# Optimization experiments

Measured on AMD Instinct MI355X. Metric: run time of the kernel, lower is better.

The kernel has to match this reference:

```python
import jax, jax.numpy as jnp
import numpy as np

N = 64
K_CHEB = 5
EPS = 1e-5

# db4 decomposition filters (scaling_filter.mat Lo_D / Hi_D, length 8)
_LO = np.array([-0.010597401784997278, 0.032883011666982945, 0.030841381835986965,
                -0.18703481171888114, -0.02798376941698385, 0.6308807679295904,
                0.7148465705525415, 0.23037781330885523], dtype=np.float32)
_HI = np.array([-0.23037781330885523, 0.7148465705525415, -0.6308807679295904,
                -0.02798376941698385, 0.18703481171888114, 0.030841381835986965,
                0.032883011666982945, -0.010597401784997278], dtype=np.float32)
# torch stores np.flip(filters) and Conv2d does cross-correlation -> use flipped taps here too
_KERN = np.stack([_LO[::-1], _HI[::-1]])[:, None, None, :].copy()  # [2,1,1,8]


def _wavelet_step(x):
    # x: [B, C, 1, W]; circular pad 3 each side, depthwise len-8 conv, stride 2
    p = 3  # filter_length // 2 - 1
    xp = jnp.concatenate([x[..., -p:], x, x[..., :p]], axis=-1)
    b, c, h, wp = xp.shape
    out = jax.lax.conv_general_dilated(
        xp.reshape(b * c, 1, h, wp), jnp.asarray(_KERN), (1, 2), 'VALID',
        dimension_numbers=('NCHW', 'OIHW', 'NCHW'))
    out = out.reshape(b, c, 2, h, -1)
    return out[:, :, 0], out[:, :, 1]  # (approx, detail)


def _cbam(x, fc1, fc2, sa_w):
    # x: [B, 657, 1, 64]; channel attention then spatial attention
    def mlp(v):  # v: [B, C, 1, 1]
        h = jax.nn.relu(jnp.einsum('oc,bchw->bohw', fc1, v))
        return jnp.einsum('oc,bchw->bohw', fc2, h)
    avg = x.mean(axis=(2, 3), keepdims=True)
    mx = x.max(axis=(2, 3), keepdims=True)
    x = x * jax.nn.sigmoid(mlp(avg) + mlp(mx))
    s = jnp.concatenate([x.mean(axis=1, keepdims=True), x.max(axis=1, keepdims=True)], axis=1)
    sa = jax.nn.sigmoid(jax.lax.conv_general_dilated(
        s, sa_w, (1, 1), ((3, 3), (3, 3)), dimension_numbers=('NCHW', 'OIHW', 'NCHW')))
    return x * sa


def _global_edge_weight(w_tril, mask):
    xs, ys = np.tril_indices(N)
    E = jnp.zeros((N, N), w_tril.dtype).at[xs, ys].set(w_tril)
    E = E + E.T - jnp.diag(jnp.diag(E))
    return (E * mask).reshape(-1)


def _norm_adj(edges, w):
    # PyG NewSGConv.norm: add remaining self-loops (fill=1), deg from |w|, sym normalize
    row, col = edges[0], edges[1]
    has_self = jnp.zeros((N,), w.dtype).at[row].add(jnp.where(row == col, 1.0, 0.0)) > 0
    w_self = jnp.where(has_self, 0.0, 1.0).astype(w.dtype)
    deg = jnp.zeros((N,), w.dtype).at[row].add(jnp.abs(w)) + w_self
    dsafe = jnp.where(deg > 0, deg, 1.0)
    dinv = jnp.where(deg > 0, jax.lax.rsqrt(dsafe), 0.0)
    norm = dinv[row] * w * dinv[col]
    A = jnp.zeros((N, N), w.dtype).at[col, row].add(norm)  # out[i] = sum_j A[i,j] x[j]
    return A + jnp.diag(dinv * w_self * dinv)


def _gcn_block(x, A, W, b, g, be):
    # x: [B, N, C_in]; K-hop SGConv propagation, linear, train-mode batchnorm over (B, N)
    for _ in range(K_CHEB):
        x = jnp.einsum('ij,bjc->bic', A, x)
    x = x @ W.T + b
    mean = x.mean(axis=(0, 1))
    var = x.var(axis=(0, 1))
    return (x - mean) * jax.lax.rsqrt(var + EPS) * g + be


def _classify(x, W1, b1, g, be, W2, b2):
    out = x.reshape(x.shape[0], -1) @ W1.T + b1
    out = (out - out.mean(0)) * jax.lax.rsqrt(out.var(0) + EPS) * g + be
    return jax.nn.log_softmax(out @ W2.T + b2, axis=1)


def _forward(x, local_graph_weight, global_mask, ca_fc1, ca_fc2, sa_conv, edge_weight_tril,
             ld_W, ld_b, ld_g, ld_be, ld1_W, ld1_b, ld1_g, ld1_be,
             d_W, d_b, d_g, d_be, d1_W, d1_b, d1_g, d1_be,
             cls_W1, cls_b1, cls_g, cls_be, cls_W2, cls_b2, edges):
    xc = jnp.transpose(x, (0, 3, 2, 1))        # [B, 657, 1, 64]
    xc = _cbam(xc, ca_fc1, ca_fc2, sa_conv)
    xh = jnp.transpose(xc, (0, 3, 2, 1))       # [B, 64, 1, 657]
    # fi = floor(log2(200)) = 7 -> 4 decomposition levels: 657->328->164->82->41
    out1, _gamma = _wavelet_step(xh)
    out2, _beta = _wavelet_step(out1)
    out3, _alpha = _wavelet_step(out2)
    delta, _theta = _wavelet_step(out3)        # [B, 64, 1, 41]
    delta = delta[:, :, 0, :]                  # squeeze -> [B, 64, 41]
    gw = _global_edge_weight(edge_weight_tril, global_mask)
    A_loc = _norm_adj(edges, local_graph_weight)
    A_glb = _norm_adj(edges, gw)
    lf = _gcn_block(delta, A_loc, ld_W, ld_b, ld_g, ld_be)
    lf = _gcn_block(lf, A_loc, ld1_W, ld1_b, ld1_g, ld1_be)
    gf = _gcn_block(delta, A_glb, d_W, d_b, d_g, d_be)
    gf = _gcn_block(gf, A_glb, d1_W, d1_b, d1_g, d1_be)
    feat = jnp.concatenate([lf.mean(-1, keepdims=True), gf.mean(-1, keepdims=True)], axis=2)  # [B,64,2]
    return _classify(feat, cls_W1, cls_b1, cls_g, cls_be, cls_W2, cls_b2)


def setup_inputs() -> dict:
    key = jax.random.key(0)
    ks = iter(jax.random.split(key, 16))
    B = 512
    f32 = jnp.float32
    def rn(shape, s=0.05):
        return jax.random.normal(next(ks), shape, f32) * s
    ii = jnp.arange(N, dtype=jnp.int32)
    edges = jnp.stack([jnp.repeat(ii, N), jnp.tile(ii, N)])  # full 64x64 mesh (incl. self loops)
    return dict(
        x=jax.random.normal(next(ks), (B, N, 1, 657), f32),
        local_graph_weight=jax.random.uniform(next(ks), (N * N,), f32),
        global_mask=jnp.ones((N, N), f32),
        ca_fc1=rn((82, 657)),
        ca_fc2=rn((657, 82)),
        sa_conv=rn((1, 2, 7, 7), 0.1),
        edge_weight_tril=jax.random.uniform(next(ks), (N * (N + 1) // 2,), f32),
        ld_W=rn((16, 41)), ld_b=jnp.zeros(16, f32), ld_g=jnp.ones(16, f32), ld_be=jnp.zeros(16, f32),
        ld1_W=rn((4, 16)), ld1_b=jnp.zeros(4, f32), ld1_g=jnp.ones(4, f32), ld1_be=jnp.zeros(4, f32),
        d_W=rn((16, 41)), d_b=jnp.zeros(16, f32), d_g=jnp.ones(16, f32), d_be=jnp.zeros(16, f32),
        d1_W=rn((4, 16)), d1_b=jnp.zeros(4, f32), d1_g=jnp.ones(4, f32), d1_be=jnp.zeros(4, f32),
        cls_W1=rn((32, 128)), cls_b1=jnp.zeros(32, f32), cls_g=jnp.ones(32, f32), cls_be=jnp.zeros(32, f32),
        cls_W2=rn((2, 32)), cls_b2=jnp.zeros(2, f32),
        edges=edges,
    )


def reference(x, local_graph_weight, global_mask, ca_fc1, ca_fc2, sa_conv, edge_weight_tril,
              ld_W, ld_b, ld_g, ld_be, ld1_W, ld1_b, ld1_g, ld1_be,
              d_W, d_b, d_g, d_be, d1_W, d1_b, d1_g, d1_be,
              cls_W1, cls_b1, cls_g, cls_be, cls_W2, cls_b2, edges):
    return _forward(x, local_graph_weight, global_mask, ca_fc1, ca_fc2, sa_conv, edge_weight_tril,
                    ld_W, ld_b, ld_g, ld_be, ld1_W, ld1_b, ld1_g, ld1_be,
                    d_W, d_b, d_g, d_be, d1_W, d1_b, d1_g, d1_be,
                    cls_W1, cls_b1, cls_g, cls_be, cls_W2, cls_b2, edges)
```

## Files before the change

kernel.cpp:

```cpp
#include <hip/hip_runtime.h>
#include <math.h>

#define NB 512
#define NN 64
#define TL 657
#define LV1 328
#define LV2 164
#define LV3 82
#define LV4 41
#define HID 82
#define ST 66

#define WS_M      0
#define WS_ACC    32768
#define WS_SMEAN  36864
#define WS_SMAX   167936
#define WS_FC2T   299008
#define WS_CSUM   682496
#define WS_CMAX   2028032
#define WS_CATT   3373568
#define WS_Y1     682496
#define WS_DELTA  4876800
#define WS_Y2     4876800
#define WS_OUT1   5925376

#define ACC_Y1 0
#define ACC_Y2 64
#define ACC_O1 80

__device__ __forceinline__ float sigmoidf_(float v){ return 1.0f/(1.0f+expf(-v)); }

__device__ __forceinline__ void wav_level(float* __restrict__ dst, const float* __restrict__ src,
                                          int outL, int inL, int lane){
  const float DLO[8] = {0.23037781330885523f, 0.7148465705525415f, 0.6308807679295904f,
                        -0.02798376941698385f, -0.18703481171888114f, 0.030841381835986965f,
                        0.032883011666982945f, -0.010597401784997278f};
  for (int k=lane; k<outL; k+=64){
    int i0 = 2*k - 3;
    float a = 0.f;
    #pragma unroll
    for (int j=0;j<8;j++){
      int idx = i0 + j;
      idx = (idx < 0) ? idx + inL : ((idx >= inL) ? idx - inL : idx);
      a += src[idx]*DLO[j];
    }
    dst[k] = a;
  }
}

__device__ __forceinline__ void mm8(float* __restrict__ D, int dstride,
                                    const float* __restrict__ A, const float* __restrict__ Bm){
  int tid = threadIdx.x;
  int wv = tid >> 6, lane = tid & 63;
  int i0 = wv*8;
  float acc8[8];
  #pragma unroll
  for (int i=0;i<8;i++) acc8[i]=0.f;
  #pragma unroll
  for (int kc=0; kc<4; kc++){
    float bb[16];
    #pragma unroll
    for (int j=0;j<16;j++) bb[j] = Bm[(kc*16+j)*ST + lane];
    #pragma unroll
    for (int i=0;i<8;i++){
      const float2* ar = (const float2*)&A[(i0+i)*ST + kc*16];
      float s0=0.f, s1=0.f;
      #pragma unroll
      for (int j2=0;j2<8;j2++){
        float2 v = ar[j2];
        s0 += v.x*bb[2*j2]; s1 += v.y*bb[2*j2+1];
      }
      acc8[i] += s0+s1;
    }
  }
  #pragma unroll
  for (int i=0;i<8;i++) D[(i0+i)*dstride + lane] = acc8[i];
}

__global__ __launch_bounds__(512) void k_front(
    const float* __restrict__ x,
    const float* __restrict__ lgw, const float* __restrict__ gmask,
    const float* __restrict__ tril, const int* __restrict__ edges,
    const float* __restrict__ fc2,
    float* __restrict__ csum, float* __restrict__ cmax,
    float* __restrict__ Mout, float* __restrict__ fc2T,
    double* __restrict__ acc)
{
  __shared__ float smem[3*NN*ST];
  __shared__ float deg[64], hs[64], dinv[64], wself[64];
  int tid = threadIdx.x;
  int bid = blockIdx.x;

  if (bid < 2*NB){
    int b = bid >> 1, band = bid & 1;
    int c0   = band ? 329 : 0;
    int len  = band ? 328 : 329;
    if (tid >= len) return;
    int col = c0 + tid;
    const float* p = x + (size_t)b*NN*TL + col;
    float s = 0.f, m = -INFINITY;
    for (int n=0;n<NN;n+=16){
      float v0 = p[0*TL],  v1 = p[1*TL],  v2 = p[2*TL],  v3 = p[3*TL];
      float v4 = p[4*TL],  v5 = p[5*TL],  v6 = p[6*TL],  v7 = p[7*TL];
      float v8 = p[8*TL],  v9 = p[9*TL],  vA = p[10*TL], vB = p[11*TL];
      float vC = p[12*TL], vD = p[13*TL], vE = p[14*TL], vF = p[15*TL];
      p += 16*TL;
      s += ((v0+v1)+(v2+v3)) + ((v4+v5)+(v6+v7)) + ((v8+v9)+(vA+vB)) + ((vC+vD)+(vE+vF));
      float m01 = fmaxf(fmaxf(v0,v1), fmaxf(v2,v3));
      float m23 = fmaxf(fmaxf(v4,v5), fmaxf(v6,v7));
      float m45 = fmaxf(fmaxf(v8,v9), fmaxf(vA,vB));
      float m67 = fmaxf(fmaxf(vC,vD), fmaxf(vE,vF));
      m = fmaxf(m, fmaxf(fmaxf(m01,m23), fmaxf(m45,m67)));
    }
    csum[(size_t)b*TL + col] = s;
    cmax[(size_t)b*TL + col] = m;
    return;
  }

  int gi = bid - 2*NB;
  if (gi >= 2){
    int t8 = gi - 2;
    int r0 = t8*83;
    int rn = (t8==7) ? (TL - 7*83) : 83;
    for (int i=tid; i<rn*HID; i+=512){
      int r = i / HID, u = i - r*HID;
      smem[u*85 + r] = fc2[(size_t)r0*HID + i];
    }
    __syncthreads();
    for (int j=tid; j<HID*83; j+=512){
      int u = j / 83, c = j - u*83;
      if (c < rn) fc2T[u*TL + r0 + c] = smem[u*85 + c];
    }
    return;
  }

  float* Wbuf = smem;
  float* Amat = smem + NN*ST;
  float* P1   = smem + 2*NN*ST;
  int g = gi;
  if (g==0 && tid<512) acc[tid]=0.0;
  for (int e=tid;e<4096;e+=512){
    float w;
    if (g==0) w = lgw[e];
    else {
      int i=e>>6, j=e&63;
      int aa = (i>j)? i:j, bb = (i>j)? j:i;
      w = tril[aa*(aa+1)/2 + bb] * gmask[e];
    }
    Wbuf[e] = w;
  }
  for (int i=tid;i<NN*ST;i+=512) Amat[i] = 0.f;
  if (tid<64){ deg[tid]=0.f; hs[tid]=0.f; }
  __syncthreads();
  {
    int e0 = tid*8;
    int runr = edges[e0];
    float runv = 0.f;
    #pragma unroll 4
    for (int i=0;i<8;i++){
      int e = e0+i;
      int r = edges[e];
      int c = edges[4096+e];
      float w = Wbuf[e];
      if (r != runr){ atomicAdd(&deg[runr], runv); runr = r; runv = 0.f; }
      runv += fabsf(w);
      if (r == c) hs[r] = 1.f;
    }
    atomicAdd(&deg[runr], runv);
  }
  __syncthreads();
  if (tid<64){
    float w_ = (hs[tid] > 0.f) ? 0.f : 1.f;
    float d = deg[tid] + w_;
    dinv[tid] = (d > 0.f) ? rsqrtf(d) : 0.f;
    wself[tid] = w_;
  }
  __syncthreads();
  for (int e=tid;e<4096;e+=512){
    int r = edges[e], c = edges[4096+e];
    float nm = dinv[r]*Wbuf[e]*dinv[c];
    atomicAdd(&Amat[c*ST+r], nm);
  }
  __syncthreads();
  if (tid<64) Amat[tid*ST+tid] += dinv[tid]*wself[tid]*dinv[tid];
  __syncthreads();
  mm8(P1,   ST, Amat, Amat); __syncthreads();
  mm8(Wbuf, ST, P1,   P1);   __syncthreads();
  mm8(&Mout[g*4096], 64, Wbuf, Amat);
}

__global__ __launch_bounds__(512) void k_mlp(
    const float* __restrict__ csum, const float* __restrict__ cmax,
    const float* __restrict__ fc1, const float* __restrict__ fc2T,
    float* __restrict__ catt)
{
  __shared__ float cs[TL], cm[TL];
  __shared__ float h[HID];
  int tid = threadIdx.x, b = blockIdx.x;
  for (int i=tid;i<TL;i+=512){
    cs[i] = csum[(size_t)b*TL + i];
    cm[i] = cmax[(size_t)b*TL + i];
  }
  __syncthreads();
  int wv = tid>>6, lane = tid&63;
  for (int o=wv; o<HID; o+=8){
    const float* fr = fc1 + (size_t)o*TL;
    float a = 0.f, bm = 0.f;
    #pragma unroll
    for (int i=0;i<11;i++){
      int c = lane + 64*i;
      if (c < TL){
        float f = fr[c];
        a += f*cs[c]; bm += f*cm[c];
      }
    }
    #pragma unroll
    for (int off=32;off;off>>=1){
      a  += __shfl_xor(a,off);
      bm += __shfl_xor(bm,off);
    }
    if (lane==0)
      h[o] = fmaxf(a*(1.0f/64.0f),0.f) + fmaxf(bm,0.f);
  }
  __syncthreads();
  for (int c=tid;c<TL;c+=512){
    float a=0.f;
    #pragma unroll 4
    for (int u=0;u<HID;u++) a += fc2T[(size_t)u*TL + c]*h[u];
    catt[(size_t)b*TL + c] = sigmoidf_(a);
  }
}

__global__ __launch_bounds__(256) void k_wav(
    const float* __restrict__ x, const float* __restrict__ catt_g,
    float* __restrict__ delta, float* __restrict__ smean, float* __restrict__ smax)
{
  __shared__ float catt[TL];
  __shared__ float yb[4][TL];
  __shared__ float o1b[4][LV1];
  __shared__ float o2b[4][LV2];
  __shared__ float o3b[4][LV3];
  int tid = threadIdx.x, b = blockIdx.x;
  for (int i=tid;i<TL;i+=256) catt[i] = catt_g[(size_t)b*TL + i];
  __syncthreads();
  int wv = tid>>6, lane = tid&63;
  int n = blockIdx.y*4 + wv;
  float* y  = yb[wv];
  float* p1 = o1b[wv];
  float* p2 = o2b[wv];
  float* p3 = o3b[wv];
  const float DLO[8] = {0.23037781330885523f, 0.7148465705525415f, 0.6308807679295904f,
                        -0.02798376941698385f, -0.18703481171888114f, 0.030841381835986965f,
                        0.032883011666982945f, -0.010597401784997278f};
  const float* row = x + ((size_t)b*NN + n)*TL;
  float ls = 0.f, lm = -INFINITY;
  #pragma unroll
  for (int i=0;i<11;i++){
    int t = lane + 64*i;
    if (t < TL){
      float v = row[t]*catt[t];
      y[t] = v; ls += v; lm = fmaxf(lm,v);
    }
  }
  #pragma unroll
  for (int off=32;off;off>>=1){
    ls += __shfl_xor(ls,off);
    lm = fmaxf(lm, __shfl_xor(lm,off));
  }
  if (lane==0){ smean[b*NN+n] = ls*(1.0f/657.0f); smax[b*NN+n] = lm; }
  wav_level(p1, y,  LV1, TL,  lane);
  wav_level(p2, p1, LV2, LV1, lane);
  wav_level(p3, p2, LV3, LV2, lane);
  if (lane < LV4){
    int i0 = 2*lane - 3;
    float a = 0.f;
    #pragma unroll
    for (int j=0;j<8;j++){
      int idx = i0 + j;
      idx = (idx < 0) ? idx + LV3 : ((idx >= LV3) ? idx - LV3 : idx);
      a += p3[idx]*DLO[j];
    }
    delta[((size_t)b*NN + n)*LV4 + lane] = a;
  }
}

__global__ __launch_bounds__(256) void k_gcn1(
  const float* __restrict__ delta, const float* __restrict__ Mmat,
  const float* __restrict__ smean, const float* __restrict__ smax,
  const float* __restrict__ saw,
  const float* __restrict__ ldW, const float* __restrict__ ldb,
  const float* __restrict__ dW, const float* __restrict__ db2,
  float* __restrict__ Y1, double* __restrict__ acc)
{
  __shared__ float Dl[NN*LV4];
  __shared__ float Tt[NN*16];
  __shared__ float Mm[4096];
  __shared__ float Wl[16*LV4];
  __shared__ float satt[NN];
  __shared__ double red[256];
  int tid=threadIdx.x, b=blockIdx.x;
  if (tid < NN){
    float a = 0.f;
    #pragma unroll
    for (int kw=0;kw<7;kw++){
      int w = tid + kw - 3;
      if (0<=w && w<NN) a += smean[b*NN+w]*saw[21+kw] + smax[b*NN+w]*saw[70+kw];
    }
    satt[tid] = sigmoidf_(a);
  }
  __syncthreads();
  const float* ds = delta + (size_t)b*NN*LV4;
  for (int i=tid;i<NN*LV4;i+=256) Dl[i] = ds[i]*satt[i/LV4];
  for (int g=0; g<2; g++){
    const float* Ws = g ? dW : ldW;
    const float* bs = g ? db2 : ldb;
    for (int i=tid;i<16*LV4;i+=256) Wl[i]=Ws[i];
    for (int i=tid;i<4096;i+=256) Mm[i]=Mmat[g*4096+i];
    __syncthreads();
    for (int e=tid;e<NN*16;e+=256){
      int n=e>>4, o=e&15;
      const float* dr=&Dl[n*LV4];
      const float* wr=&Wl[o*LV4];
      float a=0.f;
      #pragma unroll 8
      for (int c=0;c<LV4;c++) a += dr[c]*wr[c];
      Tt[e]=a;
    }
    __syncthreads();
    float bias = bs[tid&15];
    float ps=0.f, pq=0.f;
    for (int m=0;m<4;m++){
      int e=tid+256*m;
      int n=e>>4, o=e&15;
      float a=bias;
      #pragma unroll 8
      for (int k=0;k<64;k++) a += Mm[n*64+k]*Tt[k*16+o];
      Y1[((size_t)b*NN+n)*32 + g*16 + o] = a;
      ps += a; pq += a*a;
    }
    red[tid]=(double)ps;
    __syncthreads();
    if (tid<16){ double t=0; for (int r=tid;r<256;r+=16) t+=red[r]; atomicAdd(&acc[ACC_Y1+g*32+tid], t); }
    __syncthreads();
    red[tid]=(double)pq;
    __syncthreads();
    if (tid<16){ double t=0; for (int r=tid;r<256;r+=16) t+=red[r]; atomicAdd(&acc[ACC_Y1+g*32+16+tid], t); }
    __syncthreads();
  }
}

__global__ __launch_bounds__(256) void k_gcn2(
  const float* __restrict__ Y1, const float* __restrict__ Mmat,
  const float* __restrict__ ldg, const float* __restrict__ ldbe,
  const float* __restrict__ dg, const float* __restrict__ dbe,
  const float* __restrict__ ld1W, const float* __restrict__ ld1b,
  const float* __restrict__ d1W, const float* __restrict__ d1b,
  float* __restrict__ Y2, double* __restrict__ acc)
{
  __shared__ float Yl[NN*32];
  __shared__ float T2[NN*8];
  __shared__ float Mm[2*4096];
  __shared__ float scl[32], sht[32];
  __shared__ double red[256];
  int tid=threadIdx.x, b=blockIdx.x;
  const float* ys = Y1 + (size_t)b*NN*32;
  for (int i=tid;i<NN*32;i+=256) Yl[i]=ys[i];
  for (int i=tid;i<8192;i+=256) Mm[i]=Mmat[i];
  if (tid<32){
    int g=tid>>4, o=tid&15;
    double s=acc[ACC_Y1+g*32+o], q=acc[ACC_Y1+g*32+16+o];
    double mean=s/32768.0;
    double var=q/32768.0 - mean*mean;
    float gam = g? dg[o] : ldg[o];
    float bet = g? dbe[o] : ldbe[o];
    float sc = gam * rsqrtf((float)var + 1e-5f);
    scl[tid]=sc; sht[tid]=bet - (float)mean*sc;
  }
  __syncthreads();
  for (int i=tid;i<NN*32;i+=256){ int c=i&31; Yl[i]=Yl[i]*scl[c]+sht[c]; }
  __syncthreads();
  for (int e=tid;e<NN*8;e+=256){
    int n=e>>3, c=e&7, g=c>>2, p=c&3;
    const float* w = (g? d1W : ld1W) + p*16;
    const float* yr = &Yl[n*32 + g*16];
    float a=0.f;
    #pragma unroll
    for (int o=0;o<16;o++) a += yr[o]*w[o];
    T2[e]=a;
  }
  __syncthreads();
  float ps=0.f,pq=0.f;
  for (int m=0;m<2;m++){
    int e=tid+256*m;
    int n=e>>3, c=e&7, g=c>>2;
    float a = g? d1b[c&3] : ld1b[c&3];
    const float* mr=&Mm[g*4096+n*64];
    #pragma unroll 8
    for (int k=0;k<64;k++) a += mr[k]*T2[k*8+c];
    Y2[((size_t)b*NN+n)*8 + c] = a;
    ps+=a; pq+=a*a;
  }
  red[tid]=(double)ps; __syncthreads();
  if (tid<8){ double t=0; for (int r=tid;r<256;r+=8) t+=red[r]; atomicAdd(&acc[ACC_Y2 + (tid>>2)*8 + (tid&3)], t); }
  __syncthreads();
  red[tid]=(double)pq; __syncthreads();
  if (tid<8){ double t=0; for (int r=tid;r<256;r+=8) t+=red[r]; atomicAdd(&acc[ACC_Y2 + (tid>>2)*8 + 4 + (tid&3)], t); }
}

__global__ __launch_bounds__(64) void k_featcls(
  const float* __restrict__ Y2,
  const float* __restrict__ ld1g, const float* __restrict__ ld1be,
  const float* __restrict__ d1g, const float* __restrict__ d1be,
  const float* __restrict__ W1, const float* __restrict__ b1,
  float* __restrict__ out1, double* __restrict__ acc)
{
  __shared__ float f[128];
  __shared__ float scl[8], sht[8];
  int tid=threadIdx.x, b=blockIdx.x;
  if (tid<8){
    int g=tid>>2, p=tid&3;
    double s=acc[ACC_Y2+g*8+p], q=acc[ACC_Y2+g*8+4+p];
    double mean=s/32768.0;
    double var=q/32768.0-mean*mean;
    float gam = g? d1g[p]:ld1g[p];
    float bet = g? d1be[p]:ld1be[p];
    float sc = gam*rsqrtf((float)var+1e-5f);
    scl[tid]=sc; sht[tid]=bet-(float)mean*sc;
  }
  __syncthreads();
  {
    const float* yr = Y2 + ((size_t)b*NN+tid)*8;
    float lf=0.f, gf=0.f;
    #pragma unroll
    for (int p=0;p<4;p++){
      lf += yr[p]*scl[p]+sht[p];
      gf += yr[4+p]*scl[4+p]+sht[4+p];
    }
    f[2*tid]   = lf*0.25f;
    f[2*tid+1] = gf*0.25f;
  }
  __syncthreads();
  if (tid<32){
    const float* w = W1 + tid*128;
    float a = b1[tid];
    #pragma unroll 4
    for (int m=0;m<128;m++) a += w[m]*f[m];
    out1[b*32+tid]=a;
    atomicAdd(&acc[ACC_O1+tid], (double)a);
    atomicAdd(&acc[ACC_O1+32+tid], (double)(a*a));
  }
}

__global__ __launch_bounds__(64) void k_cls2(
  const float* __restrict__ out1,
  const float* __restrict__ cg, const float* __restrict__ cbe,
  const float* __restrict__ W2, const float* __restrict__ b2,
  const double* __restrict__ acc, float* __restrict__ out)
{
  __shared__ float v[32];
  __shared__ float z[2];
  int tid=threadIdx.x, b=blockIdx.x;
  if (tid<32){
    double s=acc[ACC_O1+tid], q=acc[ACC_O1+32+tid];
    double mean=s/512.0;
    double var=q/512.0-mean*mean;
    float sc=cg[tid]*rsqrtf((float)var+1e-5f);
    float sh=cbe[tid]-(float)mean*sc;
    v[tid]=out1[b*32+tid]*sc+sh;
  }
  __syncthreads();
  if (tid<2){
    const float* w=W2+tid*32;
    float a=b2[tid];
    #pragma unroll
    for (int j=0;j<32;j++) a += w[j]*v[j];
    z[tid]=a;
  }
  __syncthreads();
  if (tid<2){
    float m=fmaxf(z[0],z[1]);
    float l=m+logf(expf(z[0]-m)+expf(z[1]-m));
    out[b*2+tid]=z[tid]-l;
  }
}

extern "C" void kernel_launch(void* const* d_in, const int* in_sizes, int n_in,
                              void* d_out, int out_size, void* d_ws, size_t ws_size,
                              hipStream_t stream) {
  (void)in_sizes; (void)n_in; (void)out_size; (void)ws_size;
  const float* x     = (const float*)d_in[0];
  const float* lgw   = (const float*)d_in[1];
  const float* gmask = (const float*)d_in[2];
  const float* fc1   = (const float*)d_in[3];
  const float* fc2   = (const float*)d_in[4];
  const float* saw   = (const float*)d_in[5];
  const float* tril  = (const float*)d_in[6];
  const float* ldW   = (const float*)d_in[7];
  const float* ldb   = (const float*)d_in[8];
  const float* ldg   = (const float*)d_in[9];
  const float* ldbe  = (const float*)d_in[10];
  const float* ld1W  = (const float*)d_in[11];
  const float* ld1b  = (const float*)d_in[12];
  const float* ld1g  = (const float*)d_in[13];
  const float* ld1be = (const float*)d_in[14];
  const float* dW    = (const float*)d_in[15];
  const float* db2   = (const float*)d_in[16];
  const float* dg    = (const float*)d_in[17];
  const float* dbe   = (const float*)d_in[18];
  const float* d1W   = (const float*)d_in[19];
  const float* d1b   = (const float*)d_in[20];
  const float* d1g   = (const float*)d_in[21];
  const float* d1be  = (const float*)d_in[22];
  const float* cW1   = (const float*)d_in[23];
  const float* cb1   = (const float*)d_in[24];
  const float* cgam  = (const float*)d_in[25];
  const float* cbet  = (const float*)d_in[26];
  const float* cW2   = (const float*)d_in[27];
  const float* cb2   = (const float*)d_in[28];
  const int*   edges = (const int*)d_in[29];

  char* ws = (char*)d_ws;
  float*  M     = (float*)(ws + WS_M);
  double* acc   = (double*)(ws + WS_ACC);
  float*  smean = (float*)(ws + WS_SMEAN);
  float*  smax  = (float*)(ws + WS_SMAX);
  float*  fc2T  = (float*)(ws + WS_FC2T);
  float*  csum  = (float*)(ws + WS_CSUM);
  float*  cmax  = (float*)(ws + WS_CMAX);
  float*  catt  = (float*)(ws + WS_CATT);
  float*  Y1    = (float*)(ws + WS_Y1);
  float*  delta = (float*)(ws + WS_DELTA);
  float*  Y2    = (float*)(ws + WS_Y2);
  float*  out1  = (float*)(ws + WS_OUT1);
  float*  out   = (float*)d_out;

  k_front<<<2*NB + 10, 512, 0, stream>>>(x, lgw, gmask, tril, edges, fc2,
                                         csum, cmax, M, fc2T, acc);
  k_mlp<<<NB, 512, 0, stream>>>(csum, cmax, fc1, fc2T, catt);
  k_wav<<<dim3(NB, 16), 256, 0, stream>>>(x, catt, delta, smean, smax);
  k_gcn1<<<NB, 256, 0, stream>>>(delta, M, smean, smax, saw, ldW, ldb, dW, db2, Y1, acc);
  k_gcn2<<<NB, 256, 0, stream>>>(Y1, M, ldg, ldbe, dg, dbe, ld1W, ld1b, d1W, d1b, Y2, acc);
  k_featcls<<<NB, 64, 0, stream>>>(Y2, ld1g, ld1be, d1g, d1be, cW1, cb1, out1, acc);
  k_cls2<<<NB, 64, 0, stream>>>(out1, cgam, cbet, cW2, cb2, acc, out);
}
```

Before: 183.0 us.

## Reduce channel sum/max with one block per batch and shared-memory tree

```diff
diff --git a/kernel.cpp b/kernel.cpp
--- a/kernel.cpp
+++ b/kernel.cpp
@@ -91,33 +91,59 @@
   int tid = threadIdx.x;
   int bid = blockIdx.x;
 
-  if (bid < 2*NB){
-    int b = bid >> 1, band = bid & 1;
-    int c0   = band ? 329 : 0;
-    int len  = band ? 328 : 329;
-    if (tid >= len) return;
-    int col = c0 + tid;
-    const float* p = x + (size_t)b*NN*TL + col;
-    float s = 0.f, m = -INFINITY;
-    for (int n=0;n<NN;n+=16){
-      float v0 = p[0*TL],  v1 = p[1*TL],  v2 = p[2*TL],  v3 = p[3*TL];
-      float v4 = p[4*TL],  v5 = p[5*TL],  v6 = p[6*TL],  v7 = p[7*TL];
-      float v8 = p[8*TL],  v9 = p[9*TL],  vA = p[10*TL], vB = p[11*TL];
-      float vC = p[12*TL], vD = p[13*TL], vE = p[14*TL], vF = p[15*TL];
-      p += 16*TL;
-      s += ((v0+v1)+(v2+v3)) + ((v4+v5)+(v6+v7)) + ((v8+v9)+(vA+vB)) + ((vC+vD)+(vE+vF));
-      float m01 = fmaxf(fmaxf(v0,v1), fmaxf(v2,v3));
-      float m23 = fmaxf(fmaxf(v4,v5), fmaxf(v6,v7));
-      float m45 = fmaxf(fmaxf(v8,v9), fmaxf(vA,vB));
-      float m67 = fmaxf(fmaxf(vC,vD), fmaxf(vE,vF));
-      m = fmaxf(m, fmaxf(fmaxf(m01,m23), fmaxf(m45,m67)));
-    }
-    csum[(size_t)b*TL + col] = s;
-    cmax[(size_t)b*TL + col] = m;
+  if (bid < NB){
+    int b = bid;
+    int wv = tid>>6, lane = tid&63;
+    float s[11], m[11];
+    #pragma unroll
+    for (int i=0;i<11;i++){ s[i]=0.f; m[i]=-INFINITY; }
+    const float* xb = x + (size_t)b*NN*TL;
+    for (int r=0;r<8;r++){
+      const float* row = xb + (size_t)(wv*8 + r)*TL;
+      #pragma unroll
+      for (int i=0;i<11;i++){
+        int t = lane + 64*i;
+        if (t < TL){
+          float v = row[t];
+          s[i] += v; m[i] = fmaxf(m[i], v);
+        }
+      }
+    }
+    float* buf = smem;
+    for (int step=4; step>=1; step>>=1){
+      if (wv >= step && wv < 2*step){
+        float* bs = buf + (wv-step)*2*664;
+        #pragma unroll
+        for (int i=0;i<11;i++){
+          int t = lane + 64*i;
+          if (t<TL){ bs[t] = s[i]; bs[664+t] = m[i]; }
+        }
+      }
+      __syncthreads();
+      if (wv < step){
+        float* bs = buf + wv*2*664;
+        #pragma unroll
+        for (int i=0;i<11;i++){
+          int t = lane + 64*i;
+          if (t<TL){ s[i] += bs[t]; m[i] = fmaxf(m[i], bs[664+t]); }
+        }
+      }
+      __syncthreads();
+    }
+    if (wv==0){
+      #pragma unroll
+      for (int i=0;i<11;i++){
+        int t = lane + 64*i;
+        if (t<TL){
+          csum[(size_t)b*TL + t] = s[i];
+          cmax[(size_t)b*TL + t] = m[i];
+        }
+      }
+    }
     return;
   }
 
-  int gi = bid - 2*NB;
+  int gi = bid - NB;
   if (gi >= 2){
     int t8 = gi - 2;
     int r0 = t8*83;
@@ -534,8 +560,8 @@
   float*  out1  = (float*)(ws + WS_OUT1);
   float*  out   = (float*)d_out;
 
-  k_front<<<2*NB + 10, 512, 0, stream>>>(x, lgw, gmask, tril, edges, fc2,
-                                         csum, cmax, M, fc2T, acc);
+  k_front<<<NB + 10, 512, 0, stream>>>(x, lgw, gmask, tril, edges, fc2,
+                                       csum, cmax, M, fc2T, acc);
   k_mlp<<<NB, 512, 0, stream>>>(csum, cmax, fc1, fc2T, catt);
   k_wav<<<dim3(NB, 16), 256, 0, stream>>>(x, catt, delta, smean, smax);
   k_gcn1<<<NB, 256, 0, stream>>>(delta, M, smean, smax, saw, ldW, ldb, dW, db2, Y1, acc);
```

After: 184.1 us. No clear change (+0.6%).
